# Kernel tuning notes

Measured on AMD Instinct MI355X. Metric: run time of the kernel, lower is better.

The kernel has to match this reference:

```python
import jax, jax.numpy as jnp
import numpy as np
from jax import lax

K, D = 7, 2                      # kernel_size, dilation
PAD = (K - 1) * D                # = 12, matches init padding
B, CIN, COUT, L = 8, 128, 256, 4096


def _na_indices(L2, k, d):
    """NATTEN-style dilated 1D neighborhood: key positions + rel-pos-bias indices."""
    i = jnp.arange(L2)
    r, ii = i % d, i // d
    Lg = (L2 - r + d - 1) // d                       # dilation-group lengths
    start = jnp.clip(ii - k // 2, 0, Lg - k)         # clamped window start (in-group)
    t = jnp.arange(k)
    pos = r[:, None] + d * (start[:, None] + t[None, :])        # [L2,k] key positions
    bidx = start[:, None] + t[None, :] - ii[:, None] + (k - 1)  # [L2,k] rpb index in [0,2k-2]
    return pos, bidx


def setup_inputs() -> dict:
    key = jax.random.key(0)
    ks = jax.random.split(key, 11)
    s = 0.05
    return {
        "x": jax.random.normal(ks[0], (B, CIN, L), jnp.float32),
        "conv1_v": jax.random.normal(ks[1], (COUT, CIN, K), jnp.float32) * s,
        "conv1_g": jax.random.uniform(ks[2], (COUT,), jnp.float32, 0.5, 1.5),
        "conv1_b": jax.random.normal(ks[3], (COUT,), jnp.float32) * s,
        "qkv_w": jax.random.normal(ks[4], (3 * COUT, COUT), jnp.float32) * s,
        "qkv_b": jax.random.normal(ks[5], (3 * COUT,), jnp.float32) * s,
        "rpb": jax.random.normal(ks[6], (1, 2 * K - 1), jnp.float32) * s,
        "proj_w": jax.random.normal(ks[7], (COUT, COUT), jnp.float32) * s,
        "proj_b": jax.random.normal(ks[8], (COUT,), jnp.float32) * s,
        "ds_w": jax.random.normal(ks[9], (COUT, CIN, 1), jnp.float32) * s,
        "ds_b": jax.random.normal(ks[10], (COUT,), jnp.float32) * s,
    }


def reference(x, conv1_v, conv1_g, conv1_b, qkv_w, qkv_b, rpb, proj_w, proj_b, ds_w, ds_b):
    # weight_norm: w = g * v / ||v|| over (in_ch, kernel) per out channel
    vn = jnp.sqrt(jnp.sum(conv1_v * conv1_v, axis=(1, 2), keepdims=True))
    w1 = conv1_g[:, None, None] * conv1_v / vn
    out = lax.conv_general_dilated(x, w1, (1,), [(PAD, PAD)], rhs_dilation=(D,),
                                   dimension_numbers=("NCH", "OIH", "NCH"))
    out = out + conv1_b[None, :, None]
    out = jax.nn.relu(out[:, :, :-PAD])              # chomp1 + relu (dropout = eval identity)

    # left-pad then neighborhood attention on [B, L2, C]
    h = jnp.pad(out, ((0, 0), (0, 0), (PAD, 0))).transpose(0, 2, 1)
    L2 = h.shape[1]
    qkv = h @ qkv_w.T + qkv_b
    q, k_, v = jnp.split(qkv, 3, axis=-1)            # single head, head_dim = COUT
    pos, bidx = _na_indices(L2, K, D)
    kg = k_[:, pos, :]                               # [B, L2, K, C]
    vg = v[:, pos, :]
    scores = jnp.einsum("blc,blkc->blk", q * (COUT ** -0.5), kg) + rpb[0][bidx][None]
    attn = jax.nn.softmax(scores, axis=-1)
    o = jnp.einsum("blk,blkc->blc", attn, vg) @ proj_w.T + proj_b

    out = jax.nn.relu(o.transpose(0, 2, 1)[:, :, :-PAD])   # chomp2 + relu
    res = jnp.einsum("bcl,oc->bol", x, ds_w[:, :, 0]) + ds_b[None, :, None]
    return jax.nn.relu(out + res)
```

## Files before the change

kernel.cpp:

```cpp
#include <hip/hip_runtime.h>
#include <math.h>

#define KW 7
#define PADW 12
#define BATCH 8
#define CIN 128
#define COUT 256
#define LEN 4096
#define L2V 4108
#define KCONV 896
#define PTILE 128

typedef unsigned short u16;
typedef short v8s __attribute__((ext_vector_type(8)));
typedef float v4f __attribute__((ext_vector_type(4)));

#define KEY3(r) ((((r) & 3) ^ (((r) >> 2) & 1)))

__device__ __forceinline__ u16 f2bf(float f) {
  unsigned int x = __float_as_uint(f);
  x += 0x7fffu + ((x >> 16) & 1u);
  return (u16)(x >> 16);
}
__device__ __forceinline__ float bf2f(u16 u) {
  return __uint_as_float(((unsigned int)u) << 16);
}

__device__ __forceinline__ void gll16(const void* g, void* l) {
  __builtin_amdgcn_global_load_lds(
      (const __attribute__((address_space(1))) void*)g,
      (__attribute__((address_space(3))) void*)l, 16, 0, 0);
}

__device__ __forceinline__ void wait_vm(int n) {
  switch (n) {
    case 0: asm volatile("s_waitcnt vmcnt(0)" ::: "memory"); break;
    case 2: asm volatile("s_waitcnt vmcnt(2)" ::: "memory"); break;
    case 3: asm volatile("s_waitcnt vmcnt(3)" ::: "memory"); break;
  }
}
#define LGKM0()  asm volatile("s_waitcnt lgkmcnt(0)" ::: "memory")
#define BARRIER() { __builtin_amdgcn_s_barrier(); asm volatile("" ::: "memory"); }

#define MFMA16(ACC, AA, BB)                                                    \
  { _Pragma("unroll") for (int fi_ = 0; fi_ < 4; ++fi_)                        \
    _Pragma("unroll") for (int fj_ = 0; fj_ < 4; ++fj_)                        \
      ACC[fi_][fj_] = __builtin_amdgcn_mfma_f32_16x16x32_bf16(                 \
          AA[fi_], BB[fj_], ACC[fi_][fj_], 0, 0, 0); }

__global__ __launch_bounds__(256) void prep_wn(
    const float* __restrict__ v, const float* __restrict__ g,
    u16* __restrict__ wt)
{
  const int c = blockIdx.x;
  const float* vo = v + (size_t)c * (CIN * KW);
  float s = 0.f;
  for (int i = threadIdx.x; i < CIN * KW; i += 256) { float t = vo[i]; s += t * t; }
#pragma unroll
  for (int off = 1; off < 64; off <<= 1) s += __shfl_xor(s, off);
  __shared__ float red[4];
  if ((threadIdx.x & 63) == 0) red[threadIdx.x >> 6] = s;
  __syncthreads();
  const float tot = red[0] + red[1] + red[2] + red[3];
  const float scale = g[c] / sqrtf(tot);
  for (int i = threadIdx.x; i < CIN * KW; i += 256) {
    const int ci = i / 7, t = i - ci * 7;
    wt[((size_t)c * KW + t) * CIN + ci] = f2bf(vo[i] * scale);
  }
}

__global__ __launch_bounds__(256) void prep_fold(
    const float* __restrict__ qw, const float* __restrict__ pw,
    u16* __restrict__ gwb, u16* __restrict__ mpv)
{
  const int z = blockIdx.z;
  const int d0 = blockIdx.y * 64, c0 = blockIdx.x * 64;
  const int tid = threadIdx.x;
  const int tx = tid & 15, ty = tid >> 4;
  __shared__ float As[16][68], Bs[16][68];
  float acc[4][4] = {};
  const int idx = tid * 4;
  const int kk4 = idx >> 6, cc4 = idx & 63;
  const int lm = idx >> 4, lk = idx & 15;

  for (int k0 = 0; k0 < 256; k0 += 16) {
    if (z == 0) {
      *(float4*)&As[kk4][cc4] = *(const float4*)(qw + (size_t)(256 + k0 + kk4) * 256 + d0 + cc4);
      *(float4*)&Bs[kk4][cc4] = *(const float4*)(qw + (size_t)(k0 + kk4) * 256 + c0 + cc4);
    } else {
      const float4 va = *(const float4*)(pw + (size_t)(d0 + lm) * 256 + k0 + lk);
      As[lk + 0][lm] = va.x; As[lk + 1][lm] = va.y; As[lk + 2][lm] = va.z; As[lk + 3][lm] = va.w;
      *(float4*)&Bs[kk4][cc4] = *(const float4*)(qw + (size_t)(512 + k0 + kk4) * 256 + c0 + cc4);
    }
    __syncthreads();
#pragma unroll
    for (int kk = 0; kk < 16; ++kk) {
      const float4 a = *(const float4*)&As[kk][ty * 4];
      const float4 bb = *(const float4*)&Bs[kk][tx * 4];
      const float av[4] = {a.x, a.y, a.z, a.w}, bv[4] = {bb.x, bb.y, bb.z, bb.w};
#pragma unroll
      for (int i = 0; i < 4; ++i)
#pragma unroll
        for (int j = 0; j < 4; ++j) acc[i][j] += av[i] * bv[j];
    }
    __syncthreads();
  }
  u16* dst = z ? mpv : gwb;
  const float scale = z ? 1.f : 0.0625f;
#pragma unroll
  for (int i = 0; i < 4; ++i) {
    const int d = d0 + ty * 4 + i;
#pragma unroll
    for (int j = 0; j < 4; ++j)
      dst[(size_t)d * 256 + c0 + tx * 4 + j] = f2bf(acc[i][j] * scale);
  }
}

__global__ __launch_bounds__(256) void fold_misc(
    const float* __restrict__ qw, const float* __restrict__ qb,
    const float* __restrict__ pw, const float* __restrict__ pb,
    const float* __restrict__ dw, float* __restrict__ params,
    u16* __restrict__ dwb)
{
  const int bid = blockIdx.x, tid = threadIdx.x;
  if (bid >= 258) {
    const int i = (bid - 258) * 256 + tid;
    dwb[i] = f2bf(dw[i]);
    return;
  }
  if (bid >= 2) {
    const int o = bid - 2;
    float part = pw[(size_t)o * 256 + tid] * qb[512 + tid];
#pragma unroll
    for (int off = 1; off < 64; off <<= 1) part += __shfl_xor(part, off);
    __shared__ float red[4];
    if ((tid & 63) == 0) red[tid >> 6] = part;
    __syncthreads();
    if (tid == 0) params[512 + o] = red[0] + red[1] + red[2] + red[3] + pb[o];
    return;
  }
  if (bid == 1) {
    float s0 = 0, s1 = 0, s2 = 0, s3 = 0;
    for (int a = 0; a < 256; a += 4) {
      s0 += qw[(size_t)(a + 0) * 256 + tid] * qb[256 + a + 0];
      s1 += qw[(size_t)(a + 1) * 256 + tid] * qb[256 + a + 1];
      s2 += qw[(size_t)(a + 2) * 256 + tid] * qb[256 + a + 2];
      s3 += qw[(size_t)(a + 3) * 256 + tid] * qb[256 + a + 3];
    }
    params[256 + tid] = 0.0625f * (s0 + s1 + s2 + s3);
    return;
  }
  float s0 = 0, s1 = 0, s2 = 0, s3 = 0;
  for (int a = 0; a < 256; a += 4) {
    s0 += qw[(size_t)(256 + a + 0) * 256 + tid] * qb[a + 0];
    s1 += qw[(size_t)(256 + a + 1) * 256 + tid] * qb[a + 1];
    s2 += qw[(size_t)(256 + a + 2) * 256 + tid] * qb[a + 2];
    s3 += qw[(size_t)(256 + a + 3) * 256 + tid] * qb[a + 3];
  }
  params[tid] = 0.0625f * (s0 + s1 + s2 + s3);
  float part = qb[tid] * qb[256 + tid];
#pragma unroll
  for (int off = 1; off < 64; off <<= 1) part += __shfl_xor(part, off);
  __shared__ float red2[4];
  if ((tid & 63) == 0) red2[tid >> 6] = part;
  __syncthreads();
  if (tid == 0) params[768] = 0.0625f * (red2[0] + red2[1] + red2[2] + red2[3]);
}

__global__ __launch_bounds__(256) void zero_fill2(
    u16* __restrict__ xT, u16* __restrict__ h, u16* __restrict__ g,
    const float* __restrict__ params)
{
  const int idx = blockIdx.x * 256 + threadIdx.x;
  if (idx < 12288) {
    const int b = idx / 1536, r = idx - b * 1536;
    xT[(size_t)b * L2V * CIN + r] = 0;
  } else if (idx < 36864) {
    const int k = idx - 12288;
    const int b = k / 3072, r = k - b * 3072;
    h[(size_t)b * L2V * COUT + r] = 0;
  } else {
    const int k = idx - 36864;
    const int b = k / 3072, r = k - b * 3072;
    g[(size_t)b * L2V * COUT + r] = f2bf(params[r & 255]);
  }
}

__global__ __launch_bounds__(256) void xpose(const float* __restrict__ x, u16* __restrict__ xT)
{
  const int b = blockIdx.y, p0 = blockIdx.x * 64;
  const int tx = threadIdx.x & 15, ty = threadIdx.x >> 4;
  const int p = p0 + ty * 4;
  const float* xb = x + (size_t)b * CIN * LEN;
  u16* xTb = xT + (size_t)b * L2V * CIN + (size_t)(PADW + p) * CIN;
#pragma unroll
  for (int half = 0; half < 2; ++half) {
    const int ci0 = half * 64 + tx * 4;
    float r[4][4];
#pragma unroll
    for (int i = 0; i < 4; ++i)
      *(float4*)r[i] = *(const float4*)(xb + (size_t)(ci0 + i) * LEN + p);
#pragma unroll
    for (int j = 0; j < 4; ++j)
      *(ushort4*)(xTb + (size_t)j * CIN + ci0) =
          make_ushort4(f2bf(r[0][j]), f2bf(r[1][j]), f2bf(r[2][j]), f2bf(r[3][j]));
  }
}

__global__ __launch_bounds__(512, 2) void conv_g_fused(
    const u16* __restrict__ wt, const u16* __restrict__ xT,
    const float* __restrict__ c1b, const u16* __restrict__ gwb,
    const float* __restrict__ params, u16* __restrict__ hout,
    u16* __restrict__ gout)
{
  const int b = blockIdx.y;
  const int p0 = blockIdx.x * PTILE;
  const int tid = threadIdx.x;
  const int w = tid >> 6, lane = tid & 63;
  const int l15 = lane & 15, kg = lane >> 4;
  const int wA = w >> 1, wB = w & 1;

  __shared__ u16 hA[PTILE * 256];
  __shared__ u16 pool[40960];

  const u16* xTb = xT + (size_t)b * L2V * CIN + (size_t)p0 * CIN;

  v4f acc[4][4];
#pragma unroll
  for (int i = 0; i < 4; ++i)
#pragma unroll
    for (int j = 0; j < 4; ++j) acc[i][j] = (v4f){0.f, 0.f, 0.f, 0.f};

  auto stageA = [&](int s, int buf) {
    const int t = s >> 2, ci0 = (s & 3) << 5;
    u16* dst = pool + buf * 12288;
#pragma unroll
    for (int i = 0; i < 2; ++i) {
      const int cidx = i * 512 + tid;
      const int row = cidx >> 2, ch = cidx & 3;
      gll16(wt + (size_t)row * KCONV + t * CIN + ci0 + ((ch ^ KEY3(row)) << 3),
            (void*)(dst + cidx * 8));
    }
    {
      const int row = tid >> 2, ch = tid & 3;
      gll16(xTb + (size_t)(2 * t + row) * CIN + ci0 + ((ch ^ KEY3(row)) << 3),
            (void*)(dst + 8192 + tid * 8));
    }
  };

  stageA(0, 0);
  stageA(1, 1);

#pragma unroll
  for (int s = 0; s < 28; ++s) {
    if (s < 27) wait_vm(3); else wait_vm(0);
    BARRIER()
    if (s < 26) stageA(s + 2, (s + 2) % 3);
    const u16* wbuf = pool + (s % 3) * 12288;
    const u16* xbuf = wbuf + 8192;
    v8s a[4], bb[4];
#pragma unroll
    for (int f = 0; f < 4; ++f) {
      const int c = wA * 64 + f * 16 + l15;
      a[f] = *(const v8s*)&wbuf[c * 32 + ((kg ^ KEY3(c)) << 3)];
      const int p = wB * 64 + f * 16 + l15;
      bb[f] = *(const v8s*)&xbuf[p * 32 + ((kg ^ KEY3(p)) << 3)];
    }
    MFMA16(acc, a, bb)
  }

#pragma unroll
  for (int fi = 0; fi < 4; ++fi) {
    const int cb = wA * 64 + fi * 16 + kg * 4;
    const float4 bv = *(const float4*)(c1b + cb);
    const int ch32 = cb >> 3, off = cb & 7;
#pragma unroll
    for (int fj = 0; fj < 4; ++fj) {
      const int p = wB * 64 + fj * 16 + l15;
      *(ushort4*)&hA[p * 256 + ((ch32 ^ (p & 7)) << 3) + off] = make_ushort4(
          f2bf(fmaxf(acc[fi][fj][0] + bv.x, 0.f)),
          f2bf(fmaxf(acc[fi][fj][1] + bv.y, 0.f)),
          f2bf(fmaxf(acc[fi][fj][2] + bv.z, 0.f)),
          f2bf(fmaxf(acc[fi][fj][3] + bv.w, 0.f)));
      acc[fi][fj] = (v4f){0.f, 0.f, 0.f, 0.f};
    }
  }
  LGKM0();
  BARRIER()

  const size_t mg0h = (size_t)b * L2V + PADW + p0;
#pragma unroll
  for (int i = 0; i < 8; ++i) {
    const int chunk = i * 512 + tid;
    const int p = chunk >> 5, ci = chunk & 31;
    const int4 vv = *(const int4*)&hA[p * 256 + ((ci ^ (p & 7)) << 3)];
    *(int4*)(hout + (mg0h + p) * COUT + ci * 8) = vv;
  }

  auto stageB = [&](int s, int buf) {
    u16* dst = pool + buf * 8192;
#pragma unroll
    for (int i = 0; i < 2; ++i) {
      const int cidx = i * 512 + tid;
      const int row = cidx >> 2, ch = cidx & 3;
      gll16(gwb + (size_t)row * COUT + (s << 5) + ((ch ^ KEY3(row)) << 3),
            (void*)(dst + cidx * 8));
    }
  };
  stageB(0, 0);
  stageB(1, 1);

#pragma unroll
  for (int s = 0; s < 8; ++s) {
    if (s < 7) wait_vm(2); else wait_vm(0);
    BARRIER()
    if (s < 6) stageB(s + 2, (s + 2) % 3);
    const u16* nbuf = pool + (s % 3) * 8192;
    v8s a[4], bb[4];
#pragma unroll
    for (int f = 0; f < 4; ++f) {
      const int n = wA * 64 + f * 16 + l15;
      a[f] = *(const v8s*)&nbuf[n * 32 + ((kg ^ KEY3(n)) << 3)];
      const int m = wB * 64 + f * 16 + l15;
      bb[f] = *(const v8s*)&hA[m * 256 + ((((s << 2) + kg) ^ (m & 7)) << 3)];
    }
    MFMA16(acc, a, bb)
  }

  u16* T = pool + 24576;
#pragma unroll
  for (int h2 = 0; h2 < 2; ++h2) {
    if ((wA >> 1) == h2) {
#pragma unroll
      for (int fi = 0; fi < 4; ++fi) {
        const int jj = (wA & 1) * 64 + fi * 16 + kg * 4;
        const float4 bv = *(const float4*)(params + h2 * 128 + jj);
        const int jc = jj >> 3, joff = jj & 7;
#pragma unroll
        for (int fj = 0; fj < 4; ++fj) {
          const int m = wB * 64 + fj * 16 + l15;
          *(ushort4*)&T[m * 128 + ((jc ^ (m & 15)) << 3) + joff] = make_ushort4(
              f2bf(acc[fi][fj][0] + bv.x), f2bf(acc[fi][fj][1] + bv.y),
              f2bf(acc[fi][fj][2] + bv.z), f2bf(acc[fi][fj][3] + bv.w));
        }
      }
    }
    LGKM0();
    BARRIER()
#pragma unroll
    for (int i2 = 0; i2 < 4; ++i2) {
      const int chunk = i2 * 512 + tid;
      const int m = chunk >> 4, j16 = chunk & 15;
      const int4 vv = *(const int4*)&T[m * 128 + ((j16 ^ (m & 15)) << 3)];
      *(int4*)(gout + (mg0h + m) * COUT + h2 * 128 + j16 * 8) = vv;
    }
    LGKM0();
    BARRIER()
  }
}

__global__ __launch_bounds__(256) void attn_v2(
    const u16* __restrict__ h, const u16* __restrict__ g,
    const float* __restrict__ params, const float* __restrict__ rpb,
    u16* __restrict__ sout)
{
  const int wid = (blockIdx.x << 2) + (threadIdx.x >> 6);
  const int lane = threadIdx.x & 63;
  const int b = wid >> 12;
  const int j = wid & 4095;
  const int r = j & 1, ii = j >> 1;
  int start = ii - 3;
  start = start < 0 ? 0 : start;
  start = start > 2047 ? 2047 : start;

  const u16* hb = h + (size_t)b * L2V * COUT;
  const u16* gb = g + (size_t)b * L2V * COUT;

  const ushort4 gv = *(const ushort4*)(gb + (size_t)j * COUT + 4 * lane);
  const float g0 = bf2f(gv.x), g1 = bf2f(gv.y), g2 = bf2f(gv.z), g3 = bf2f(gv.w);
  const ushort4 hj = *(const ushort4*)(hb + (size_t)j * COUT + 4 * lane);
  const float4 wv = *(const float4*)(params + 256 + 4 * lane);
  float e = bf2f(hj.x) * wv.x + bf2f(hj.y) * wv.y +
            bf2f(hj.z) * wv.z + bf2f(hj.w) * wv.w;
#pragma unroll
  for (int o = 1; o < 64; o <<= 1) e += __shfl_xor(e, o);
  e += params[768];

  float hp[7][4];
  float sc[7];
  float mx = -1e30f;
#pragma unroll
  for (int t = 0; t < 7; ++t) {
    const int pos = r + 2 * (start + t);
    const ushort4 hv = *(const ushort4*)(hb + (size_t)pos * COUT + 4 * lane);
    hp[t][0] = bf2f(hv.x); hp[t][1] = bf2f(hv.y);
    hp[t][2] = bf2f(hv.z); hp[t][3] = bf2f(hv.w);
    float s = g0 * hp[t][0] + g1 * hp[t][1] + g2 * hp[t][2] + g3 * hp[t][3];
#pragma unroll
    for (int o = 1; o < 64; o <<= 1) s += __shfl_xor(s, o);
    s += e + rpb[start + t - ii + 6];
    sc[t] = s;
    mx = fmaxf(mx, s);
  }
  float sum = 0.f;
#pragma unroll
  for (int t = 0; t < 7; ++t) { sc[t] = __expf(sc[t] - mx); sum += sc[t]; }
  const float inv = 1.f / sum;

  float a0 = 0.f, a1 = 0.f, a2 = 0.f, a3 = 0.f;
#pragma unroll
  for (int t = 0; t < 7; ++t) {
    const float wgt = sc[t] * inv;
    a0 += wgt * hp[t][0]; a1 += wgt * hp[t][1];
    a2 += wgt * hp[t][2]; a3 += wgt * hp[t][3];
  }
  *(ushort4*)(sout + ((size_t)(b * LEN + j)) * COUT + 4 * lane) =
      make_ushort4(f2bf(a0), f2bf(a1), f2bf(a2), f2bf(a3));
}

__global__ __launch_bounds__(256, 2) void projds_gll(
    const u16* __restrict__ ao, const u16* __restrict__ pwb,
    const float* __restrict__ pb, const u16* __restrict__ xT,
    const u16* __restrict__ dwb, const float* __restrict__ db,
    float* __restrict__ out)
{
  const int b = blockIdx.z;
  const int l0 = blockIdx.x * 128, o0 = blockIdx.y * 128;
  const int tid = threadIdx.x;
  const int w = tid >> 6, lane = tid & 63;
  const int l15 = lane & 15, kg = lane >> 4;
  const int wr = w >> 1, wc = w & 1;

  __shared__ u16 sX[2][128 * 32];
  __shared__ u16 sW[2][128 * 32];

  const int arow = tid >> 2, ach = tid & 3;
  const int akey = KEY3(arow);
  const u16* aob = ao + (size_t)b * LEN * COUT;
  const u16* xTb = xT + ((size_t)b * L2V + PADW) * CIN;

  auto stage1 = [&](int s, int buf) {
#pragma unroll
    for (int i = 0; i < 2; ++i) {
      const int row = i * 64 + arow;
      const int sl = (ach ^ akey) << 3;
      gll16(aob + (size_t)(l0 + row) * COUT + (s << 5) + sl,
            (void*)&sX[buf][(i * 256 + tid) * 8]);
      gll16(pwb + (size_t)(o0 + row) * COUT + (s << 5) + sl,
            (void*)&sW[buf][(i * 256 + tid) * 8]);
    }
  };
  auto stage2 = [&](int s, int buf) {
#pragma unroll
    for (int i = 0; i < 2; ++i) {
      const int row = i * 64 + arow;
      const int sl = (ach ^ akey) << 3;
      gll16(xTb + (size_t)(l0 + row) * CIN + (s << 5) + sl,
            (void*)&sX[buf][(i * 256 + tid) * 8]);
      gll16(dwb + (size_t)(o0 + row) * CIN + (s << 5) + sl,
            (void*)&sW[buf][(i * 256 + tid) * 8]);
    }
  };

  v4f acc[4][4];
#pragma unroll
  for (int i = 0; i < 4; ++i)
#pragma unroll
    for (int j = 0; j < 4; ++j) acc[i][j] = (v4f){0.f, 0.f, 0.f, 0.f};

  stage1(0, 0);
  __syncthreads();
  for (int ss = 0; ss < 12; ++ss) {
    const int buf = ss & 1;
    if (ss < 7) stage1(ss + 1, buf ^ 1);
    else if (ss < 11) stage2(ss - 7, buf ^ 1);
    v8s a[4], bb[4];
#pragma unroll
    for (int f = 0; f < 4; ++f) {
      const int lr = wr * 64 + f * 16 + l15;
      a[f] = *(const v8s*)&sX[buf][lr * 32 + ((kg ^ KEY3(lr)) << 3)];
      const int orr = wc * 64 + f * 16 + l15;
      bb[f] = *(const v8s*)&sW[buf][orr * 32 + ((kg ^ KEY3(orr)) << 3)];
    }
#pragma unroll
    for (int fi_ = 0; fi_ < 4; ++fi_)
#pragma unroll
      for (int fj_ = 0; fj_ < 4; ++fj_)
        acc[fi_][fj_] = __builtin_amdgcn_mfma_f32_16x16x32_bf16(
            a[fi_], bb[fj_], acc[fi_][fj_], 0, 0, 0);
    if (ss == 7) {
#pragma unroll
      for (int fj = 0; fj < 4; ++fj) {
        const float pbv = pb[o0 + wc * 64 + fj * 16 + l15];
#pragma unroll
        for (int fi = 0; fi < 4; ++fi)
#pragma unroll
          for (int jj = 0; jj < 4; ++jj)
            acc[fi][fj][jj] = fmaxf(acc[fi][fj][jj] + pbv, 0.f);
      }
    }
    __syncthreads();
  }

#pragma unroll
  for (int fj = 0; fj < 4; ++fj) {
    const int o = o0 + wc * 64 + fj * 16 + l15;
    const float dbv = db[o];
    float* orow = out + ((size_t)(b * COUT + o)) * LEN;
#pragma unroll
    for (int fi = 0; fi < 4; ++fi) {
      const int lb = l0 + wr * 64 + fi * 16 + kg * 4;
      float v0 = acc[fi][fj][0] + dbv; v0 = v0 > 0.f ? v0 : 0.f;
      float v1 = acc[fi][fj][1] + dbv; v1 = v1 > 0.f ? v1 : 0.f;
      float v2 = acc[fi][fj][2] + dbv; v2 = v2 > 0.f ? v2 : 0.f;
      float v3 = acc[fi][fj][3] + dbv; v3 = v3 > 0.f ? v3 : 0.f;
      *(float4*)(orow + lb) = make_float4(v0, v1, v2, v3);
    }
  }
}

extern "C" void kernel_launch(void* const* d_in, const int* in_sizes, int n_in,
                              void* d_out, int out_size, void* d_ws, size_t ws_size,
                              hipStream_t stream)
{
  (void)in_sizes; (void)n_in; (void)out_size; (void)ws_size;
  const float* x   = (const float*)d_in[0];
  const float* c1v = (const float*)d_in[1];
  const float* c1g = (const float*)d_in[2];
  const float* c1b = (const float*)d_in[3];
  const float* qw  = (const float*)d_in[4];
  const float* qb  = (const float*)d_in[5];
  const float* rpb = (const float*)d_in[6];
  const float* pw  = (const float*)d_in[7];
  const float* pb  = (const float*)d_in[8];
  const float* dw  = (const float*)d_in[9];
  const float* db  = (const float*)d_in[10];
  float* out = (float*)d_out;

  char* ws = (char*)d_ws;
  u16*   wt     = (u16*)(ws);
  u16*   gwb    = (u16*)(ws + 458752);
  u16*   mpv    = (u16*)(ws + 589824);
  u16*   dwb    = (u16*)(ws + 720896);
  float* params = (float*)(ws + 786432);
  u16*   xT     = (u16*)(ws + 1048576);
  u16*   h      = (u16*)(ws + 9461760);
  u16*   g      = (u16*)(ws + 26288128);
  u16*   s      = (u16*)(ws + 43114496);

  prep_wn<<<COUT, 256, 0, stream>>>(c1v, c1g, wt);
  prep_fold<<<dim3(4, 4, 2), 256, 0, stream>>>(qw, pw, gwb, mpv);
  fold_misc<<<386, 256, 0, stream>>>(qw, qb, pw, pb, dw, params, dwb);
  zero_fill2<<<240, 256, 0, stream>>>(xT, h, g, params);
  xpose<<<dim3(LEN / 64, BATCH), 256, 0, stream>>>(x, xT);
  conv_g_fused<<<dim3(LEN / PTILE, BATCH), 512, 0, stream>>>(wt, xT, c1b, gwb, params, h, g);
  attn_v2<<<(BATCH * LEN) / 4, 256, 0, stream>>>(h, g, params, rpb, s);
  projds_gll<<<dim3(LEN / 128, COUT / 128, BATCH), 256, 0, stream>>>(
      s, mpv, params + 512, xT, dwb, db, out);
}
```

Before: 112.3 us.

## Drop query-constant score terms and pack four queries per wavefront in attention

The per-query bias term e (h_j·w + const) is the same for every key in a softmax row, so it cancels out. Its computation and the fold kernels that produced it are removed. The attention kernel now maps 16 lanes per query, so one wavefront handles four queries. Each lane loads 16 bf16 channels with 128-bit loads and the reduction needs only 4 shuffle steps instead of 6. In exchange, register use per lane rises, since each lane now keeps seven 16-channel rows of h live.

New measurement: 101.9 us, median of 2. 1.1x faster.

```diff
diff --git a/kernel.cpp b/kernel.cpp
--- a/kernel.cpp
+++ b/kernel.cpp
@@ -139,17 +139,7 @@
     if (tid == 0) params[512 + o] = red[0] + red[1] + red[2] + red[3] + pb[o];
     return;
   }
-  if (bid == 1) {
-    float s0 = 0, s1 = 0, s2 = 0, s3 = 0;
-    for (int a = 0; a < 256; a += 4) {
-      s0 += qw[(size_t)(a + 0) * 256 + tid] * qb[256 + a + 0];
-      s1 += qw[(size_t)(a + 1) * 256 + tid] * qb[256 + a + 1];
-      s2 += qw[(size_t)(a + 2) * 256 + tid] * qb[256 + a + 2];
-      s3 += qw[(size_t)(a + 3) * 256 + tid] * qb[256 + a + 3];
-    }
-    params[256 + tid] = 0.0625f * (s0 + s1 + s2 + s3);
-    return;
-  }
+  if (bid == 1) return;
   float s0 = 0, s1 = 0, s2 = 0, s3 = 0;
   for (int a = 0; a < 256; a += 4) {
     s0 += qw[(size_t)(256 + a + 0) * 256 + tid] * qb[a + 0];
@@ -158,13 +148,6 @@
     s3 += qw[(size_t)(256 + a + 3) * 256 + tid] * qb[a + 3];
   }
   params[tid] = 0.0625f * (s0 + s1 + s2 + s3);
-  float part = qb[tid] * qb[256 + tid];
-#pragma unroll
-  for (int off = 1; off < 64; off <<= 1) part += __shfl_xor(part, off);
-  __shared__ float red2[4];
-  if ((tid & 63) == 0) red2[tid >> 6] = part;
-  __syncthreads();
-  if (tid == 0) params[768] = 0.0625f * (red2[0] + red2[1] + red2[2] + red2[3]);
 }
 
 __global__ __launch_bounds__(256) void zero_fill2(
@@ -359,15 +342,16 @@
   }
 }
 
-__global__ __launch_bounds__(256) void attn_v2(
+__global__ __launch_bounds__(256) void attn_v3(
     const u16* __restrict__ h, const u16* __restrict__ g,
-    const float* __restrict__ params, const float* __restrict__ rpb,
-    u16* __restrict__ sout)
-{
-  const int wid = (blockIdx.x << 2) + (threadIdx.x >> 6);
+    const float* __restrict__ rpb, u16* __restrict__ sout)
+{
+  const int wid = blockIdx.x * 4 + (threadIdx.x >> 6);
   const int lane = threadIdx.x & 63;
-  const int b = wid >> 12;
-  const int j = wid & 4095;
+  const int sub = lane >> 4, cg = lane & 15;
+  const int q = wid * 4 + sub;
+  const int b = q >> 12;
+  const int j = q & 4095;
   const int r = j & 1, ii = j >> 1;
   int start = ii - 3;
   start = start < 0 ? 0 : start;
@@ -375,30 +359,42 @@
 
   const u16* hb = h + (size_t)b * L2V * COUT;
   const u16* gb = g + (size_t)b * L2V * COUT;
-
-  const ushort4 gv = *(const ushort4*)(gb + (size_t)j * COUT + 4 * lane);
-  const float g0 = bf2f(gv.x), g1 = bf2f(gv.y), g2 = bf2f(gv.z), g3 = bf2f(gv.w);
-  const ushort4 hj = *(const ushort4*)(hb + (size_t)j * COUT + 4 * lane);
-  const float4 wv = *(const float4*)(params + 256 + 4 * lane);
-  float e = bf2f(hj.x) * wv.x + bf2f(hj.y) * wv.y +
-            bf2f(hj.z) * wv.z + bf2f(hj.w) * wv.w;
-#pragma unroll
-  for (int o = 1; o < 64; o <<= 1) e += __shfl_xor(e, o);
-  e += params[768];
-
-  float hp[7][4];
+  const int co = cg * 16;
+
+  float gf[16];
+  {
+    const int4 g0 = *(const int4*)(gb + (size_t)j * COUT + co);
+    const int4 g1 = *(const int4*)(gb + (size_t)j * COUT + co + 8);
+    const int gw[8] = {g0.x, g0.y, g0.z, g0.w, g1.x, g1.y, g1.z, g1.w};
+#pragma unroll
+    for (int i = 0; i < 8; ++i) {
+      const unsigned int u = (unsigned int)gw[i];
+      gf[2 * i]     = __uint_as_float(u << 16);
+      gf[2 * i + 1] = __uint_as_float(u & 0xffff0000u);
+    }
+  }
+
+  int4 hp0[7], hp1[7];
   float sc[7];
   float mx = -1e30f;
 #pragma unroll
   for (int t = 0; t < 7; ++t) {
     const int pos = r + 2 * (start + t);
-    const ushort4 hv = *(const ushort4*)(hb + (size_t)pos * COUT + 4 * lane);
-    hp[t][0] = bf2f(hv.x); hp[t][1] = bf2f(hv.y);
-    hp[t][2] = bf2f(hv.z); hp[t][3] = bf2f(hv.w);
-    float s = g0 * hp[t][0] + g1 * hp[t][1] + g2 * hp[t][2] + g3 * hp[t][3];
-#pragma unroll
-    for (int o = 1; o < 64; o <<= 1) s += __shfl_xor(s, o);
-    s += e + rpb[start + t - ii + 6];
+    const u16* hrow = hb + (size_t)pos * COUT + co;
+    hp0[t] = *(const int4*)(hrow);
+    hp1[t] = *(const int4*)(hrow + 8);
+    const int hw[8] = {hp0[t].x, hp0[t].y, hp0[t].z, hp0[t].w,
+                       hp1[t].x, hp1[t].y, hp1[t].z, hp1[t].w};
+    float s = 0.f;
+#pragma unroll
+    for (int i = 0; i < 8; ++i) {
+      const unsigned int u = (unsigned int)hw[i];
+      s += gf[2 * i]     * __uint_as_float(u << 16);
+      s += gf[2 * i + 1] * __uint_as_float(u & 0xffff0000u);
+    }
+    s += __shfl_xor(s, 1); s += __shfl_xor(s, 2);
+    s += __shfl_xor(s, 4); s += __shfl_xor(s, 8);
+    s += rpb[start + t - ii + 6];
     sc[t] = s;
     mx = fmaxf(mx, s);
   }
@@ -407,15 +403,28 @@
   for (int t = 0; t < 7; ++t) { sc[t] = __expf(sc[t] - mx); sum += sc[t]; }
   const float inv = 1.f / sum;
 
-  float a0 = 0.f, a1 = 0.f, a2 = 0.f, a3 = 0.f;
+  float acc[16];
+#pragma unroll
+  for (int i = 0; i < 16; ++i) acc[i] = 0.f;
 #pragma unroll
   for (int t = 0; t < 7; ++t) {
     const float wgt = sc[t] * inv;
-    a0 += wgt * hp[t][0]; a1 += wgt * hp[t][1];
-    a2 += wgt * hp[t][2]; a3 += wgt * hp[t][3];
-  }
-  *(ushort4*)(sout + ((size_t)(b * LEN + j)) * COUT + 4 * lane) =
-      make_ushort4(f2bf(a0), f2bf(a1), f2bf(a2), f2bf(a3));
+    const int hw[8] = {hp0[t].x, hp0[t].y, hp0[t].z, hp0[t].w,
+                       hp1[t].x, hp1[t].y, hp1[t].z, hp1[t].w};
+#pragma unroll
+    for (int i = 0; i < 8; ++i) {
+      const unsigned int u = (unsigned int)hw[i];
+      acc[2 * i]     += wgt * __uint_as_float(u << 16);
+      acc[2 * i + 1] += wgt * __uint_as_float(u & 0xffff0000u);
+    }
+  }
+  u16* dst = sout + ((size_t)(b * LEN + j)) * COUT + co;
+  ushort4 o0 = make_ushort4(f2bf(acc[0]), f2bf(acc[1]), f2bf(acc[2]), f2bf(acc[3]));
+  ushort4 o1 = make_ushort4(f2bf(acc[4]), f2bf(acc[5]), f2bf(acc[6]), f2bf(acc[7]));
+  ushort4 o2 = make_ushort4(f2bf(acc[8]), f2bf(acc[9]), f2bf(acc[10]), f2bf(acc[11]));
+  ushort4 o3 = make_ushort4(f2bf(acc[12]), f2bf(acc[13]), f2bf(acc[14]), f2bf(acc[15]));
+  *(ushort4*)(dst) = o0;  *(ushort4*)(dst + 4) = o1;
+  *(ushort4*)(dst + 8) = o2; *(ushort4*)(dst + 12) = o3;
 }
 
 __global__ __launch_bounds__(256, 2) void projds_gll(
@@ -554,7 +563,7 @@
   zero_fill2<<<240, 256, 0, stream>>>(xT, h, g, params);
   xpose<<<dim3(LEN / 64, BATCH), 256, 0, stream>>>(x, xT);
   conv_g_fused<<<dim3(LEN / PTILE, BATCH), 512, 0, stream>>>(wt, xT, c1b, gwb, params, h, g);
-  attn_v2<<<(BATCH * LEN) / 4, 256, 0, stream>>>(h, g, params, rpb, s);
+  attn_v3<<<(BATCH * LEN) / 16, 256, 0, stream>>>(h, g, rpb, s);
   projds_gll<<<dim3(LEN / 128, COUT / 128, BATCH), 256, 0, stream>>>(
       s, mpv, params + 512, xT, dwb, db, out);
 }
```
